# Kernel tuning notes

Measured on AMD Instinct MI355X. Metric: run time of the kernel, lower is better.

## Reference

```python
import jax, jax.numpy as jnp
import numpy as np

DIM = 1024
HEADS = 16
DIM_HEAD = 64
INNER = HEADS * DIM_HEAD
SCALE = DIM_HEAD ** -0.5


def setup_inputs() -> dict:
    key = jax.random.key(0)
    k1, k2, k3 = jax.random.split(key, 3)
    b, n = 2, 2048
    x = jax.random.normal(k1, (b, n, DIM), dtype=jnp.float32)
    mask = jnp.ones((b, n), dtype=bool)
    # to_qkv: Linear(dim, 3*inner, bias=False) stored as [dim, 3*inner]
    w_qkv = jax.random.normal(k2, (DIM, 3 * INNER), dtype=jnp.float32) * (DIM ** -0.5)
    # to_out: Linear(inner, dim, bias=False) stored as [inner, dim]
    w_out = jax.random.normal(k3, (INNER, DIM), dtype=jnp.float32) * (INNER ** -0.5)
    g = jnp.ones((DIM,), dtype=jnp.float32)  # LayerNorm gain
    return {"x": x, "mask": mask, "w_qkv": w_qkv, "w_out": w_out, "g": g}


def _layernorm(x, g):
    eps = 1e-5 if x.dtype == jnp.float32 else 1e-3
    mean = jnp.mean(x, axis=-1, keepdims=True)
    var = jnp.var(x, axis=-1, keepdims=True)  # unbiased=False
    return (x - mean) * jax.lax.rsqrt(var + eps) * g


def reference(x, mask, w_qkv, w_out, g):
    b, n, _ = x.shape
    qkv = x @ w_qkv  # [b, n, 3*inner]
    q, k, v = jnp.split(qkv, 3, axis=-1)
    # b n (h d) -> b h n d
    split_heads = lambda t: t.reshape(b, n, HEADS, DIM_HEAD).transpose(0, 2, 1, 3)
    q, k, v = split_heads(q), split_heads(k), split_heads(v)
    q = q * SCALE
    sim = jnp.einsum('bhid,bhjd->bhij', q, k)  # [b, h, n, n]
    mask_value = -jnp.finfo(sim.dtype).max
    key_mask = mask[:, None, None, :]  # b 1 1 j
    sim = jnp.where(key_mask, sim, mask_value)
    causal_mask = jnp.triu(jnp.ones((n, n), dtype=bool), k=1)
    sim = jnp.where(causal_mask, mask_value, sim)
    attn = jax.nn.softmax(sim.astype(jnp.float32), axis=-1).astype(sim.dtype)
    out = jnp.einsum('bhij,bhjd->bhid', attn, v)
    out = out.transpose(0, 2, 1, 3).reshape(b, n, INNER)  # b h n d -> b n (h d)
    out = out @ w_out
    return _layernorm(out, g)
```

## Files before the change

### kernel.cpp

```cpp
#include <hip/hip_runtime.h>
#include <hip/hip_bf16.h>


typedef __bf16 bf16_t;
typedef __bf16 bf16x8 __attribute__((ext_vector_type(8)));
typedef __bf16 bf16x4 __attribute__((ext_vector_type(4)));
typedef float  f32x4  __attribute__((ext_vector_type(4)));

#define DIMX   1024
#define HEADS  16
#define DHEAD  64
#define INNER  1024
#define SEQ    2048
#define BATCH  2
#define NROWS  (BATCH * SEQ)
#define QKV_N  (3 * INNER)
#define NQT    (SEQ / 64)
#define QK2SCALE 0.18033688011f

__device__ __forceinline__ bf16_t f2b(float f) { return (bf16_t)f; }

__device__ __forceinline__ float fexp2(float x) {
#if __has_builtin(__builtin_amdgcn_exp2f)
  return __builtin_amdgcn_exp2f(x);
#else
  return exp2f(x);
#endif
}

__device__ __forceinline__ void gload16(const bf16_t* g, bf16_t* s) {
  __builtin_amdgcn_global_load_lds(
      (const __attribute__((address_space(1))) unsigned int*)g,
      (__attribute__((address_space(3))) unsigned int*)s, 16, 0, 0);
}

__device__ __forceinline__ f32x4 mfma16(bf16x8 a, bf16x8 b, f32x4 c) {
  return __builtin_amdgcn_mfma_f32_16x16x32_bf16(a, b, c, 0, 0, 0);
}

__global__ __launch_bounds__(256)
void prep_all(const float* __restrict__ x, const float* __restrict__ w_qkv,
              const float* __restrict__ w_out, bf16_t* __restrict__ xb,
              bf16_t* __restrict__ wqkvT, bf16_t* __restrict__ woutT) {
  __shared__ float tile[32][33];
  const int bid = blockIdx.x;
  if (bid < 4096) {
    const int i = bid * 256 + threadIdx.x;
    float4 v = *(const float4*)&x[(size_t)i * 4];
    bf16x4 o;
    o[0] = f2b(v.x); o[1] = f2b(v.y); o[2] = f2b(v.z); o[3] = f2b(v.w);
    *(bf16x4*)&xb[(size_t)i * 4] = o;
    return;
  }
  const float* in; bf16_t* out; int R, C, bx, by;
  if (bid < 4096 + 3072) {
    const int t1 = bid - 4096;
    in = w_qkv; out = wqkvT; R = DIMX; C = QKV_N; bx = t1 % 96; by = t1 / 96;
  } else {
    const int t2 = bid - 7168;
    in = w_out; out = woutT; R = DIMX; C = DIMX; bx = t2 & 31; by = t2 >> 5;
  }
  const int c0 = bx * 32, r0 = by * 32;
  const int tx = threadIdx.x & 31, ty = threadIdx.x >> 5;
  #pragma unroll
  for (int i = 0; i < 32; i += 8)
    tile[ty + i][tx] = in[(size_t)(r0 + ty + i) * C + c0 + tx];
  __syncthreads();
  #pragma unroll
  for (int i = 0; i < 32; i += 8)
    out[(size_t)(c0 + ty + i) * R + r0 + tx] = f2b(tile[tx][ty + i]);
}

__global__ __launch_bounds__(256)
void gemm_qkv(const bf16_t* __restrict__ A, const bf16_t* __restrict__ Bt,
              bf16_t* __restrict__ C, bf16_t* __restrict__ vt) {
  constexpr int BK = 64, K = 1024, N = QKV_N;
  __shared__ bf16_t smem[2 * 128 * BK];
  bf16_t* As = smem;
  bf16_t* Bs = smem + 128 * BK;
  const int t = threadIdx.x;
  const int w = t >> 6, l = t & 63, lo = l & 15, hi = l >> 4;
  const int nwg = gridDim.x * gridDim.y;
  int flat = blockIdx.y * gridDim.x + blockIdx.x;
  flat = (flat & 7) * (nwg >> 3) + (flat >> 3);
  const int m0 = (flat / gridDim.x) * 128, n0 = (flat % gridDim.x) * 128;
  const int wm = (w >> 1) * 64, wn = (w & 1) * 64;
  const int sl  = l >> 3;
  const int sgc = ((l & 7) ^ sl) * 8;
  const int r7  = lo & 7;
  f32x4 acc[4][4] = {};
  for (int k0 = 0; k0 < K; k0 += BK) {
    #pragma unroll
    for (int c = 0; c < 4; ++c) {
      const int rb = w * 32 + c * 8;
      gload16(&A [(size_t)(m0 + rb + sl) * K + k0 + sgc], &As[rb * BK + l * 8]);
      gload16(&Bt[(size_t)(n0 + rb + sl) * K + k0 + sgc], &Bs[rb * BK + l * 8]);
    }
    __syncthreads();
    #pragma unroll
    for (int kk = 0; kk < 2; ++kk) {
      bf16x8 af[4], bfr[4];
      #pragma unroll
      for (int mi = 0; mi < 4; ++mi)
        af[mi] = *(const bf16x8*)&As[(wm + mi * 16 + lo) * BK +
                                     (((kk * 4 + hi) ^ r7) << 3)];
      #pragma unroll
      for (int nj = 0; nj < 4; ++nj)
        bfr[nj] = *(const bf16x8*)&Bs[(wn + nj * 16 + lo) * BK +
                                      (((kk * 4 + hi) ^ r7) << 3)];
      __builtin_amdgcn_s_setprio(1);
      #pragma unroll
      for (int mi = 0; mi < 4; ++mi)
        #pragma unroll
        for (int nj = 0; nj < 4; ++nj)
          acc[mi][nj] = mfma16(af[mi], bfr[nj], acc[mi][nj]);
      __builtin_amdgcn_s_setprio(0);
    }
    __syncthreads();
  }
  if (n0 < 2 * INNER) {
    #pragma unroll
    for (int mi = 0; mi < 4; ++mi)
      #pragma unroll
      for (int nj = 0; nj < 4; ++nj)
        #pragma unroll
        for (int r = 0; r < 4; ++r)
          C[(size_t)(m0 + wm + mi * 16 + hi * 4 + r) * N +
            n0 + wn + nj * 16 + lo] = f2b(acc[mi][nj][r]);
  } else {
    #pragma unroll
    for (int mi = 0; mi < 4; ++mi)
      #pragma unroll
      for (int nj = 0; nj < 4; ++nj) {
        const int cloc = wn + nj * 16 + lo;
        const int g    = ((wm + mi * 16) >> 2) + hi;
        bf16x4 pk;
        #pragma unroll
        for (int r = 0; r < 4; ++r) pk[r] = f2b(acc[mi][nj][r]);
        *(bf16x4*)((char*)smem + cloc * 256 + (((g ^ (cloc & 31))) << 3)) = pk;
      }
    __syncthreads();
    const int b  = m0 >> 11;
    const int j0 = m0 & (SEQ - 1);
    const int vrb = b * 1024 + (n0 - 2 * INNER);
    const int jb32 = (lo >> 2) * 32;
    const int pA   = (lo & 1) * 16 + ((lo >> 1) & 1) * 4;
    #pragma unroll
    for (int p = 0; p < 8; ++p) {
      const int c = p * 16 + w * 4 + hi;
      const int c31 = c & 31;
      bf16x4 a0 = *(const bf16x4*)((const char*)smem + c * 256 +
                                   (((2 * lo) ^ c31) << 3));
      bf16x4 a1 = *(const bf16x4*)((const char*)smem + c * 256 +
                                   (((2 * lo + 1) ^ c31) << 3));
      *(bf16x4*)&vt[(size_t)(vrb + c) * SEQ + j0 + jb32 + pA]     = a0;
      *(bf16x4*)&vt[(size_t)(vrb + c) * SEQ + j0 + jb32 + pA + 8] = a1;
    }
  }
}

__global__ __launch_bounds__(256)
void gemm_osk(const bf16_t* __restrict__ A0, const bf16_t* __restrict__ Bt0,
              bf16_t* __restrict__ P) {
  constexpr int BK = 64, KH = 512, LDA = 1024, N = DIMX, M = NROWS;
  __shared__ bf16_t smem[2 * 128 * BK];
  bf16_t* As = smem;
  bf16_t* Bs = smem + 128 * BK;
  const int ks = blockIdx.z;
  const bf16_t* A  = A0  + ks * KH;
  const bf16_t* Bt = Bt0 + ks * KH;
  bf16_t* Cp = P + (size_t)ks * M * N;
  const int t = threadIdx.x;
  const int w = t >> 6, l = t & 63, lo = l & 15, hi = l >> 4;
  const int nwg = gridDim.x * gridDim.y;
  int flat = blockIdx.y * gridDim.x + blockIdx.x;
  flat = (flat & 7) * (nwg >> 3) + (flat >> 3);
  const int m0 = (flat / gridDim.x) * 128, n0 = (flat % gridDim.x) * 128;
  const int wm = (w >> 1) * 64, wn = (w & 1) * 64;
  const int sl  = l >> 3;
  const int sgc = ((l & 7) ^ sl) * 8;
  const int r7  = lo & 7;
  f32x4 acc[4][4] = {};
  for (int k0 = 0; k0 < KH; k0 += BK) {
    #pragma unroll
    for (int c = 0; c < 4; ++c) {
      const int rb = w * 32 + c * 8;
      gload16(&A [(size_t)(m0 + rb + sl) * LDA + k0 + sgc], &As[rb * BK + l * 8]);
      gload16(&Bt[(size_t)(n0 + rb + sl) * LDA + k0 + sgc], &Bs[rb * BK + l * 8]);
    }
    __syncthreads();
    #pragma unroll
    for (int kk = 0; kk < 2; ++kk) {
      bf16x8 af[4], bfr[4];
      #pragma unroll
      for (int mi = 0; mi < 4; ++mi)
        af[mi] = *(const bf16x8*)&As[(wm + mi * 16 + lo) * BK +
                                     (((kk * 4 + hi) ^ r7) << 3)];
      #pragma unroll
      for (int nj = 0; nj < 4; ++nj)
        bfr[nj] = *(const bf16x8*)&Bs[(wn + nj * 16 + lo) * BK +
                                      (((kk * 4 + hi) ^ r7) << 3)];
      __builtin_amdgcn_s_setprio(1);
      #pragma unroll
      for (int mi = 0; mi < 4; ++mi)
        #pragma unroll
        for (int nj = 0; nj < 4; ++nj)
          acc[mi][nj] = mfma16(af[mi], bfr[nj], acc[mi][nj]);
      __builtin_amdgcn_s_setprio(0);
    }
    __syncthreads();
  }
  #pragma unroll
  for (int mi = 0; mi < 4; ++mi)
    #pragma unroll
    for (int nj = 0; nj < 4; ++nj)
      #pragma unroll
      for (int r = 0; r < 4; ++r)
        Cp[(size_t)(m0 + wm + mi * 16 + hi * 4 + r) * N +
           n0 + wn + nj * 16 + lo] = f2b(acc[mi][nj][r]);
}

__global__ __launch_bounds__(256, 4)
void attn_fa17(const bf16_t* __restrict__ qkv, const bf16_t* __restrict__ vt,
               bf16_t* __restrict__ attn_out, bf16_t* __restrict__ pacc,
               float* __restrict__ plsum) {
  const int bx = blockIdx.x;
  int role, bh, ta;
  {
    const int seg = bx < 512 ? 0 : (bx < 1024 ? 1 : 2);
    const int i3  = bx & 511;
    const int xcd = i3 & 7, j = i3 >> 3;
    bh = xcd * 4 + (j & 3);
    const int tq = j >> 2;
    role = seg;
    ta = (seg == 1) ? (15 - tq) : tq;
  }
  const int tb = NQT - 1 - ta;
  const int b = bh >> 4, h = bh & 15;
  const int t = threadIdx.x, w = t >> 6, l = t & 63, lo = l & 15, hi = l >> 4;

  __shared__ bf16_t Ks[2][64 * 64];
  __shared__ bf16_t Vs[2][64 * 64];

  const int srow = l >> 3;
  const int sgc  = ((l & 7) ^ srow) * 8;
  const bf16_t* kbase0 = qkv + (size_t)(b * SEQ + srow) * QKV_N + INNER + h * 64 + sgc;
  const bf16_t* vbase0 = vt + ((size_t)bh * 64 + srow) * SEQ + sgc;

  auto STAGE = [&](const bf16_t* kg, const bf16_t* vg, int buf) {
    #pragma unroll
    for (int c = 0; c < 2; ++c) {
      const int rb = w * 16 + c * 8;
      gload16(kg + (size_t)rb * QKV_N, &Ks[buf][rb * 64]);
      gload16(vg + (size_t)rb * SEQ,   &Vs[buf][rb * 64]);
    }
  };

  const int r7 = lo & 7;
  bf16x8 vone8;
  #pragma unroll
  for (int i = 0; i < 8; ++i) vone8[i] = f2b(1.0f);
  f32x4 acc[4];
  f32x4 acc_l;
  const f32x4 fz = {};

  auto SEG = [&](const int qt, const int t0, const int t1, const bool dmask) {
    const size_t qb = (size_t)(b * SEQ + qt * 64 + w * 16 + lo) * QKV_N + h * 64;
    bf16x8 qf0 = *(const bf16x8*)&qkv[qb + hi * 8];
    bf16x8 qf1 = *(const bf16x8*)&qkv[qb + 32 + hi * 8];
    #pragma unroll
    for (int i = 0; i < 8; ++i) {
      qf0[i] = f2b((float)qf0[i] * QK2SCALE);
      qf1[i] = f2b((float)qf1[i] * QK2SCALE);
    }
    acc[0] = fz; acc[1] = fz; acc[2] = fz; acc[3] = fz;
    acc_l = fz;
    const int qrow = qt * 64 + w * 16 + lo;

    const bf16_t* kg = kbase0 + (size_t)(t0 * 64) * QKV_N;
    const bf16_t* vg = vbase0 + t0 * 64;
    STAGE(kg, vg, 0);
    for (int ti = t0; ti <= t1; ++ti) {
      const int buf = (ti - t0) & 1;
      __syncthreads();
      if (ti + 1 <= t1) {
        kg += (size_t)64 * QKV_N;
        vg += 64;
        STAGE(kg, vg, buf ^ 1);
      }
      const bool mB = dmask && (ti == t1);
      __builtin_amdgcn_s_setprio(1);
      #pragma unroll
      for (int pr = 0; pr < 2; ++pr) {
        const int jb0 = pr * 2;
        if (!(mB && jb0 > w)) {
          bf16x8 pa;
          #pragma unroll
          for (int q = 0; q < 2; ++q) {
            const int jb = jb0 + q;
            f32x4 z = fz;
            if (!(mB && jb > w)) {
              const bf16_t* kp = &Ks[buf][(jb * 16 + lo) * 64];
              bf16x8 kf0 = *(const bf16x8*)&kp[(hi ^ r7) << 3];
              bf16x8 kf1 = *(const bf16x8*)&kp[((hi + 4) ^ r7) << 3];
              z = mfma16(kf0, qf0, z);
              z = mfma16(kf1, qf1, z);
            }
            #pragma unroll
            for (int r = 0; r < 4; ++r) {
              float pe = fexp2(z[r]);
              if (mB) {
                const int jglob = ti * 64 + jb * 16 + hi * 4 + r;
                if (jglob > qrow) pe = 0.f;
              }
              pa[q * 4 + r] = f2b(pe);
            }
          }
          #pragma unroll
          for (int dj = 0; dj < 4; ++dj) {
            bf16x8 vf = *(const bf16x8*)&Vs[buf][(dj * 16 + lo) * 64 +
                        (((pr * 4 + hi) ^ r7) << 3)];
            acc[dj] = mfma16(pa, vf, acc[dj]);
          }
          acc_l = mfma16(pa, vone8, acc_l);
        }
      }
      __builtin_amdgcn_s_setprio(0);
    }
    __syncthreads();
  };

  const int prb = (bh * 16 + (tb - 16)) * 64;

  if (role == 1) {
    SEG(ta, 0, ta, true);
    #pragma unroll
    for (int r = 0; r < 4; ++r) {
      const float lr = 1.f / acc_l[r];
      #pragma unroll
      for (int dj = 0; dj < 4; ++dj)
        attn_out[(size_t)(b * SEQ + ta * 64 + w * 16 + hi * 4 + r) * INNER +
                 h * 64 + dj * 16 + lo] = f2b(acc[dj][r] * lr);
    }
  } else if (role == 2) {
    SEG(tb, 0, 15 - ta, false);
    #pragma unroll
    for (int dj = 0; dj < 4; ++dj)
      #pragma unroll
      for (int r = 0; r < 4; ++r)
        pacc[(size_t)(prb + w * 16 + hi * 4 + r) * 64 + dj * 16 + lo] =
            f2b(acc[dj][r]);
    if (lo == 0) {
      #pragma unroll
      for (int r = 0; r < 4; ++r)
        plsum[prb + w * 16 + hi * 4 + r] = acc_l[r];
    }
  } else {
    SEG(tb, 16 - ta, tb, true);
    #pragma unroll
    for (int dj = 0; dj < 4; ++dj)
      #pragma unroll
      for (int r = 0; r < 4; ++r)
        pacc[2097152 + (size_t)(prb + w * 16 + hi * 4 + r) * 64 + dj * 16 + lo] =
            f2b(acc[dj][r]);
    if (lo == 0) {
      #pragma unroll
      for (int r = 0; r < 4; ++r)
        plsum[32768 + prb + w * 16 + hi * 4 + r] = acc_l[r];
    }
  }
}

__global__ __launch_bounds__(256)
void attn_combine(const bf16_t* __restrict__ pacc, const float* __restrict__ plsum,
                  bf16_t* __restrict__ attn_out) {
  const int g = blockIdx.x * 256 + threadIdx.x;
  const int d8 = g & 7;
  const int row = g >> 3;
  const int qr = row & 63, qt = 16 + ((row >> 6) & 15), bh = row >> 10;
  const int b = bh >> 4, h = bh & 15;
  bf16x8 xa = *(const bf16x8*)&pacc[(size_t)row * 64 + d8 * 8];
  bf16x8 ya = *(const bf16x8*)&pacc[2097152 + (size_t)row * 64 + d8 * 8];
  const float inv = 1.f / (plsum[row] + plsum[32768 + row]);
  bf16x8 o;
  #pragma unroll
  for (int i = 0; i < 8; ++i)
    o[i] = f2b(((float)xa[i] + (float)ya[i]) * inv);
  *(bf16x8*)&attn_out[(size_t)(b * SEQ + qt * 64 + qr) * INNER + h * 64 + d8 * 8] = o;
}

__global__ __launch_bounds__(256)
void layernorm_skb(const bf16_t* __restrict__ p0, const bf16_t* __restrict__ p1,
                   const float* __restrict__ g, float* __restrict__ out) {
  const int row = blockIdx.x;
  const int c = threadIdx.x * 4;
  bf16x4 a4 = *(const bf16x4*)&p0[(size_t)row * DIMX + c];
  bf16x4 b4 = *(const bf16x4*)&p1[(size_t)row * DIMX + c];
  const float vx = (float)a4[0] + (float)b4[0];
  const float vy = (float)a4[1] + (float)b4[1];
  const float vz = (float)a4[2] + (float)b4[2];
  const float vw = (float)a4[3] + (float)b4[3];
  float s = vx + vy + vz + vw;
  float q = vx * vx + vy * vy + vz * vz + vw * vw;
  #pragma unroll
  for (int o = 32; o > 0; o >>= 1) {
    s += __shfl_down(s, o);
    q += __shfl_down(q, o);
  }
  __shared__ float rs[4], rq[4];
  const int wid = threadIdx.x >> 6;
  if ((threadIdx.x & 63) == 0) { rs[wid] = s; rq[wid] = q; }
  __syncthreads();
  s = rs[0] + rs[1] + rs[2] + rs[3];
  q = rq[0] + rq[1] + rq[2] + rq[3];
  const float mean = s * (1.f / DIMX);
  const float var  = q * (1.f / DIMX) - mean * mean;
  const float inv  = rsqrtf(var + 1e-5f);
  float4 gv = *(const float4*)&g[c];
  float4 o4;
  o4.x = (vx - mean) * inv * gv.x;
  o4.y = (vy - mean) * inv * gv.y;
  o4.z = (vz - mean) * inv * gv.z;
  o4.w = (vw - mean) * inv * gv.w;
  *(float4*)&out[(size_t)row * DIMX + c] = o4;
}

extern "C" void kernel_launch(void* const* d_in, const int* in_sizes, int n_in,
                              void* d_out, int out_size, void* d_ws, size_t ws_size,
                              hipStream_t stream) {
  const float* x     = (const float*)d_in[0];
  const float* w_qkv = (const float*)d_in[2];
  const float* w_out = (const float*)d_in[3];
  const float* g     = (const float*)d_in[4];

  char* ws = (char*)d_ws;
  const size_t MB = 1024 * 1024;
  bf16_t* xb     = (bf16_t*)(ws);
  bf16_t* wqkvT  = (bf16_t*)(ws + 8 * MB);
  bf16_t* woutT  = (bf16_t*)(ws + 14 * MB);
  bf16_t* qkv    = (bf16_t*)(ws + 16 * MB);
  bf16_t* vt     = (bf16_t*)(ws + 40 * MB);
  bf16_t* attn_o = (bf16_t*)(ws + 48 * MB);
  bf16_t* pacc   = (bf16_t*)(ws);
  float*  plsum  = (float*) (ws + 8 * MB);
  bf16_t* partP  = (bf16_t*)(ws + 16 * MB);

  prep_all<<<8192, 256, 0, stream>>>(x, w_qkv, w_out, xb, wqkvT, woutT);

  gemm_qkv<<<dim3(QKV_N / 128, NROWS / 128), 256, 0, stream>>>(
      xb, wqkvT, qkv, vt);

  attn_fa17<<<dim3(1536), 256, 0, stream>>>(qkv, vt, attn_o, pacc, plsum);
  attn_combine<<<dim3(1024), 256, 0, stream>>>(pacc, plsum, attn_o);

  gemm_osk<<<dim3(DIMX / 128, NROWS / 128, 2), 256, 0, stream>>>(
      attn_o, woutT, partP);

  layernorm_skb<<<NROWS, 256, 0, stream>>>(
      partP, partP + (size_t)NROWS * DIMX, g, (float*)d_out);
}
```

Before: 99.54 us.

## Rebalance causal attention work split into 1280 blocks with merged short tiles

Reorganizes the causal flash-attention work decomposition: instead of three uniform roles of 512 blocks, blocks are grouped into classes ordered by workload. The longest partial segments go first, mid-length direct tiles next, and the shortest q-tiles are paired so one block handles both a small direct tile and the matching partial segment for a late tile. This reduces the block count and is meant to improve load balance and tail behaviour, at the risk of uneven per-block time in the paired class.

```diff
diff --git a/kernel.cpp b/kernel.cpp
--- a/kernel.cpp
+++ b/kernel.cpp
@@ -221,21 +221,13 @@
 }
 
 __global__ __launch_bounds__(256, 4)
-void attn_fa17(const bf16_t* __restrict__ qkv, const bf16_t* __restrict__ vt,
+void attn_fa18(const bf16_t* __restrict__ qkv, const bf16_t* __restrict__ vt,
                bf16_t* __restrict__ attn_out, bf16_t* __restrict__ pacc,
                float* __restrict__ plsum) {
   const int bx = blockIdx.x;
-  int role, bh, ta;
-  {
-    const int seg = bx < 512 ? 0 : (bx < 1024 ? 1 : 2);
-    const int i3  = bx & 511;
-    const int xcd = i3 & 7, j = i3 >> 3;
-    bh = xcd * 4 + (j & 3);
-    const int tq = j >> 2;
-    role = seg;
-    ta = (seg == 1) ? (15 - tq) : tq;
-  }
-  const int tb = NQT - 1 - ta;
+  const int xcd = bx & 7, idx = bx >> 3;
+  const int bh  = xcd * 4 + (idx & 3);
+  const int r   = idx >> 2;
   const int b = bh >> 4, h = bh & 15;
   const int t = threadIdx.x, w = t >> 6, l = t & 63, lo = l & 15, hi = l >> 4;
 
@@ -307,13 +299,13 @@
               z = mfma16(kf1, qf1, z);
             }
             #pragma unroll
-            for (int r = 0; r < 4; ++r) {
-              float pe = fexp2(z[r]);
+            for (int rr = 0; rr < 4; ++rr) {
+              float pe = fexp2(z[rr]);
               if (mB) {
-                const int jglob = ti * 64 + jb * 16 + hi * 4 + r;
+                const int jglob = ti * 64 + jb * 16 + hi * 4 + rr;
                 if (jglob > qrow) pe = 0.f;
               }
-              pa[q * 4 + r] = f2b(pe);
+              pa[q * 4 + rr] = f2b(pe);
             }
           }
           #pragma unroll
@@ -330,44 +322,51 @@
     __syncthreads();
   };
 
-  const int prb = (bh * 16 + (tb - 16)) * 64;
-
-  if (role == 1) {
+  auto STORE_DIRECT = [&](const int qt) {
+    #pragma unroll
+    for (int rr = 0; rr < 4; ++rr) {
+      const float lr = 1.f / acc_l[rr];
+      #pragma unroll
+      for (int dj = 0; dj < 4; ++dj)
+        attn_out[(size_t)(b * SEQ + qt * 64 + w * 16 + hi * 4 + rr) * INNER +
+                 h * 64 + dj * 16 + lo] = f2b(acc[dj][rr] * lr);
+    }
+  };
+  auto STORE_PART = [&](const int slab, const int tbq) {
+    const int prb = (bh * 16 + (tbq - 16)) * 64;
+    const size_t abase = (size_t)slab * 2097152;
+    #pragma unroll
+    for (int dj = 0; dj < 4; ++dj)
+      #pragma unroll
+      for (int rr = 0; rr < 4; ++rr)
+        pacc[abase + (size_t)(prb + w * 16 + hi * 4 + rr) * 64 + dj * 16 + lo] =
+            f2b(acc[dj][rr]);
+    if (lo == 0) {
+      #pragma unroll
+      for (int rr = 0; rr < 4; ++rr)
+        plsum[slab * 32768 + prb + w * 16 + hi * 4 + rr] = acc_l[rr];
+    }
+  };
+
+  if (r < 16) {
+    const int ta = r, tb = NQT - 1 - ta;
+    SEG(tb, 16 - ta, tb, true);
+    STORE_PART(1, tb);
+  } else if (r < 24) {
+    const int ta = 8 + (r - 16);
     SEG(ta, 0, ta, true);
-    #pragma unroll
-    for (int r = 0; r < 4; ++r) {
-      const float lr = 1.f / acc_l[r];
-      #pragma unroll
-      for (int dj = 0; dj < 4; ++dj)
-        attn_out[(size_t)(b * SEQ + ta * 64 + w * 16 + hi * 4 + r) * INNER +
-                 h * 64 + dj * 16 + lo] = f2b(acc[dj][r] * lr);
-    }
-  } else if (role == 2) {
+    STORE_DIRECT(ta);
+  } else if (r < 32) {
+    const int ta = r - 24, tb = NQT - 1 - ta;
     SEG(tb, 0, 15 - ta, false);
-    #pragma unroll
-    for (int dj = 0; dj < 4; ++dj)
-      #pragma unroll
-      for (int r = 0; r < 4; ++r)
-        pacc[(size_t)(prb + w * 16 + hi * 4 + r) * 64 + dj * 16 + lo] =
-            f2b(acc[dj][r]);
-    if (lo == 0) {
-      #pragma unroll
-      for (int r = 0; r < 4; ++r)
-        plsum[prb + w * 16 + hi * 4 + r] = acc_l[r];
-    }
+    STORE_PART(0, tb);
   } else {
-    SEG(tb, 16 - ta, tb, true);
-    #pragma unroll
-    for (int dj = 0; dj < 4; ++dj)
-      #pragma unroll
-      for (int r = 0; r < 4; ++r)
-        pacc[2097152 + (size_t)(prb + w * 16 + hi * 4 + r) * 64 + dj * 16 + lo] =
-            f2b(acc[dj][r]);
-    if (lo == 0) {
-      #pragma unroll
-      for (int r = 0; r < 4; ++r)
-        plsum[32768 + prb + w * 16 + hi * 4 + r] = acc_l[r];
-    }
+    const int k = r - 32;
+    SEG(k, 0, k, true);
+    STORE_DIRECT(k);
+    const int tb2 = 16 + k;
+    SEG(tb2, 0, k, false);
+    STORE_PART(0, tb2);
   }
 }
 
@@ -450,7 +449,7 @@
   gemm_qkv<<<dim3(QKV_N / 128, NROWS / 128), 256, 0, stream>>>(
       xb, wqkvT, qkv, vt);
 
-  attn_fa17<<<dim3(1536), 256, 0, stream>>>(qkv, vt, attn_o, pacc, plsum);
+  attn_fa18<<<dim3(1280), 256, 0, stream>>>(qkv, vt, attn_o, pacc, plsum);
   attn_combine<<<dim3(1024), 256, 0, stream>>>(pacc, plsum, attn_o);
 
   gemm_osk<<<dim3(DIMX / 128, NROWS / 128, 2), 256, 0, stream>>>(
```

After: 108.2 us. +8.7%, slower.
